# Performance work log

Hardware: AMD Instinct MI355X
Metric: run time of the kernel (lower is better)

The kernel has to match this reference:

```python
import jax, jax.numpy as jnp
import numpy as np

_EPSILON = 1e-6

def _sparsemax(z):
    # sparsemax along last axis. z: [b, m]
    z_sorted = -jnp.sort(-z, axis=-1)                       # descending sort
    m = z.shape[-1]
    k = jnp.arange(1, m + 1, dtype=z.dtype)                 # [m]
    z_cumsum = jnp.cumsum(z_sorted, axis=-1)                # [b, m]
    support = (1.0 + k * z_sorted) > z_cumsum               # [b, m] bool
    k_z = jnp.sum(support, axis=-1, keepdims=True)          # [b, 1] int, size of support
    cs_at_k = jnp.take_along_axis(z_cumsum, k_z - 1, axis=-1)
    tau = (cs_at_k - 1.0) / k_z.astype(z.dtype)             # threshold
    return jnp.maximum(z - tau, 0.0)


def setup_inputs() -> dict:
    key = jax.random.key(0)
    ks = jax.random.split(key, 6)
    b, m, dim, out_dim = 4096, 8192, 1024, 1000
    encoder_output = jax.random.normal(ks[0], (b, dim), dtype=jnp.float32)
    memory_set = jax.random.normal(ks[1], (m, dim), dtype=jnp.float32)
    loss_weights = jax.random.uniform(ks[2], (m, 1), dtype=jnp.float32)
    # classifier: Linear(2*dim, 4*dim) -> ReLU -> Linear(4*dim, out_dim)
    W1 = jax.random.normal(ks[3], (4 * dim, 2 * dim), dtype=jnp.float32) * (1.0 / np.sqrt(2 * dim))
    b1 = jnp.zeros((4 * dim,), dtype=jnp.float32)
    W2 = jax.random.normal(ks[4], (out_dim, 4 * dim), dtype=jnp.float32) * (1.0 / np.sqrt(4 * dim))
    b2 = jnp.zeros((out_dim,), dtype=jnp.float32)
    return {"encoder_output": encoder_output, "memory_set": memory_set,
            "loss_weights": loss_weights, "W1": W1, "b1": b1, "W2": W2, "b2": b2}


def reference(encoder_output, memory_set, loss_weights, W1, b1, W2, b2):
    # cosine distance: d = 1 - x_norm @ y_norm^T
    x_norm = encoder_output * jax.lax.rsqrt(
        jnp.sum(encoder_output * encoder_output, axis=1, keepdims=True) + _EPSILON)
    y_norm = memory_set * jax.lax.rsqrt(
        jnp.sum(memory_set * memory_set, axis=1, keepdims=True) + _EPSILON)
    d = 1.0 - jnp.matmul(x_norm, y_norm.T)                  # [b, m]
    content_weights = _sparsemax(-d)                        # [b, m], sparse rows
    memory_vector = jnp.matmul(content_weights, memory_set) # [b, dim]
    final_input = jnp.concatenate([encoder_output, memory_vector], axis=1)  # [b, 2*dim]
    h = jax.nn.relu(jnp.matmul(final_input, W1.T) + b1)
    output = jnp.matmul(h, W2.T) + b2                       # [b, out_dim]
    return output
```

## Files before the change

### kernel.cpp

```cpp
#include <hip/hip_runtime.h>

typedef __bf16 bf16;
typedef __bf16 bf16x4 __attribute__((ext_vector_type(4)));
typedef __bf16 bf16x8 __attribute__((ext_vector_type(8)));
typedef float f32x4 __attribute__((ext_vector_type(4)));
typedef _Float16 f16x8 __attribute__((ext_vector_type(8)));

#define WS_OFF_S    (0ull)
#define WS_OFF_PAIR (67108864ull)
#define WS_OFF_MB   (134217728ull)
#define WS_OFF_W1B  (150994944ull)
#define WS_OFF_W2B  (167772160ull)
#define WS_OFF_FI   (176160768ull)
#define WS_OFF_XN   (192937984ull)
#define WS_OFF_YN   (201326592ull)
#define WS_OFF_H    (0ull)
#define K_MAX 4095

__device__ __forceinline__ void gload_lds16(const void* g, void* l) {
  __builtin_amdgcn_global_load_lds(
      (const __attribute__((address_space(1))) void*)g,
      (__attribute__((address_space(3))) void*)l, 16, 0, 0);
}

template<int EPI>
__global__ __launch_bounds__(256)
void gemm_nt(const bf16* __restrict__ A, const bf16* __restrict__ B,
             void* __restrict__ Cout, const float* __restrict__ bias,
             int K, int ldc, int colLimit)
{
  __shared__ alignas(16) bf16 As[128 * 64];
  __shared__ alignas(16) bf16 Bs[128 * 64];
  const int tid  = threadIdx.x;
  const int lane = tid & 63;
  const int wave = tid >> 6;
  const int wr = wave >> 1, wc = wave & 1;
  const int bm0 = blockIdx.y << 7;
  const int bn0 = blockIdx.x << 7;

  const int lr   = lane >> 3;
  const int lcb  = (lane & 7) << 4;
  const int scolb = lcb ^ (lr << 4);
  const int row0 = (wave << 5) + lr;
  const char* Ag = (const char*)(A + (size_t)(bm0 + row0) * K) + scolb;
  const char* Bg = (const char*)(B + (size_t)(bn0 + row0) * K) + scolb;
  char* Al = (char*)As + (wave << 12);
  char* Bl = (char*)Bs + (wave << 12);
  const size_t rstride8 = (size_t)16 * K;

  int offA[2][4], offB[2][4];
  const int kb = (lane >> 4) << 4;
#pragma unroll
  for (int m = 0; m < 4; ++m) {
    const int rA = (wr << 6) + (m << 4) + (lane & 15);
    const int rB = (wc << 6) + (m << 4) + (lane & 15);
#pragma unroll
    for (int ks = 0; ks < 2; ++ks) {
      offA[ks][m] = (rA << 7) + ((((ks << 6) + kb)) ^ ((rA & 7) << 4));
      offB[ks][m] = (rB << 7) + ((((ks << 6) + kb)) ^ ((rB & 7) << 4));
    }
  }

  f32x4 acc[4][4];
#pragma unroll
  for (int m = 0; m < 4; ++m)
#pragma unroll
    for (int n = 0; n < 4; ++n) acc[m][n] = (f32x4)(0.0f);

  const char* Asb = (const char*)As;
  const char* Bsb = (const char*)Bs;
  const int nk = K >> 6;
  for (int kt = 0; kt < nk; ++kt) {
#pragma unroll
    for (int i = 0; i < 4; ++i) gload_lds16(Ag + i * rstride8, Al + (i << 10));
#pragma unroll
    for (int i = 0; i < 4; ++i) gload_lds16(Bg + i * rstride8, Bl + (i << 10));
    Ag += 128; Bg += 128;
    __syncthreads();
#pragma unroll
    for (int ks = 0; ks < 2; ++ks) {
      bf16x8 av[4], bv[4];
#pragma unroll
      for (int m = 0; m < 4; ++m) av[m] = *(const bf16x8*)(Asb + offA[ks][m]);
#pragma unroll
      for (int n = 0; n < 4; ++n) bv[n] = *(const bf16x8*)(Bsb + offB[ks][n]);
#pragma unroll
      for (int m = 0; m < 4; ++m)
#pragma unroll
        for (int n = 0; n < 4; ++n)
          acc[m][n] = __builtin_amdgcn_mfma_f32_16x16x32_bf16(av[m], bv[n], acc[m][n], 0, 0, 0);
    }
    __syncthreads();
  }

  const int r0 = bm0 + (wr << 6) + ((lane >> 4) << 2);
  const int c0 = bn0 + (wc << 6) + (lane & 15);
#pragma unroll
  for (int m = 0; m < 4; ++m) {
#pragma unroll
    for (int n = 0; n < 4; ++n) {
      const int col = c0 + (n << 4);
#pragma unroll
      for (int j = 0; j < 4; ++j) {
        const int row = r0 + (m << 4) + j;
        const float v = acc[m][n][j];
        if (EPI == 0) {
          ((_Float16*)Cout)[(size_t)row * ldc + col] = (_Float16)v;
        } else if (EPI == 2) {
          float t = v + bias[col];
          t = t > 0.f ? t : 0.f;
          ((bf16*)Cout)[(size_t)row * ldc + col] = (bf16)t;
        } else {
          if (col < colLimit)
            ((float*)Cout)[(size_t)row * ldc + col] = v + bias[col];
        }
      }
    }
  }
}

__global__ __launch_bounds__(256)
void rownorm_kernel(const float* __restrict__ X, bf16* __restrict__ XN,
                    bf16* __restrict__ RAW, int ldraw)
{
  const int row = blockIdx.x;
  const int tid = threadIdx.x;
  const float4 v = ((const float4*)(X + (size_t)row * 1024))[tid];
  float ss = v.x * v.x + v.y * v.y + v.z * v.z + v.w * v.w;
#pragma unroll
  for (int o = 32; o > 0; o >>= 1) ss += __shfl_down(ss, o);
  __shared__ float red[4];
  if ((tid & 63) == 0) red[tid >> 6] = ss;
  __syncthreads();
  const float rn = rsqrtf(red[0] + red[1] + red[2] + red[3] + 1e-6f);
  union { bf16 h[4]; unsigned long long u; } p;
  p.h[0] = (bf16)(v.x * rn); p.h[1] = (bf16)(v.y * rn);
  p.h[2] = (bf16)(v.z * rn); p.h[3] = (bf16)(v.w * rn);
  ((unsigned long long*)(XN + (size_t)row * 1024))[tid] = p.u;
  if (RAW != nullptr) {
    union { bf16 h[4]; unsigned long long u; } q;
    q.h[0] = (bf16)v.x; q.h[1] = (bf16)v.y; q.h[2] = (bf16)v.z; q.h[3] = (bf16)v.w;
    ((unsigned long long*)(RAW + (size_t)row * ldraw))[tid] = q.u;
  }
}

__global__ void cvt_bf16_kernel(const float* __restrict__ src, bf16* __restrict__ dst, int n4) {
  const int i = blockIdx.x * blockDim.x + threadIdx.x;
  if (i >= n4) return;
  const float4 v = ((const float4*)src)[i];
  union { bf16 h[4]; unsigned long long u; } p;
  p.h[0] = (bf16)v.x; p.h[1] = (bf16)v.y; p.h[2] = (bf16)v.z; p.h[3] = (bf16)v.w;
  ((unsigned long long*)dst)[i] = p.u;
}

__global__ void cvt_w2_kernel(const float* __restrict__ src, bf16* __restrict__ dst) {
  const int i = blockIdx.x * blockDim.x + threadIdx.x;
  const int row = i >> 10;
  union { bf16 h[4]; unsigned long long u; } p;
  if (row < 1000) {
    const float4 v = ((const float4*)src)[i];
    p.h[0] = (bf16)v.x; p.h[1] = (bf16)v.y; p.h[2] = (bf16)v.z; p.h[3] = (bf16)v.w;
  } else {
    p.u = 0ull;
  }
  ((unsigned long long*)dst)[i] = p.u;
}

__global__ __launch_bounds__(256)
void sparsemax_compact_kernel(const _Float16* __restrict__ S, unsigned* __restrict__ PAIRS)
{
  const int row = blockIdx.x;
  const int tid = threadIdx.x;
  const f16x8* zs = (const f16x8*)(S + (size_t)row * 8192);
  float z[32];
  float lsum = 0.f;
#pragma unroll
  for (int t = 0; t < 4; ++t) {
    const f16x8 v = zs[t * 256 + tid];
#pragma unroll
    for (int j = 0; j < 8; ++j) { const float f = (float)v[j]; z[t * 8 + j] = f; lsum += f; }
  }
  __shared__ float redS[4], redC[4];
  __shared__ int lcnt;
  if (tid == 0) lcnt = 0;
  float s = lsum;
#pragma unroll
  for (int o = 32; o > 0; o >>= 1) s += __shfl_down(s, o);
  if ((tid & 63) == 0) redS[tid >> 6] = s;
  __syncthreads();
  float tau = (redS[0] + redS[1] + redS[2] + redS[3] - 1.0f) * (1.0f / 8192.0f);

  for (int it = 0; it < 64; ++it) {
    float ls = 0.f, lc = 0.f;
#pragma unroll
    for (int j = 0; j < 32; ++j) {
      const float v = z[j];
      if (v > tau) { ls += v; lc += 1.0f; }
    }
#pragma unroll
    for (int o = 32; o > 0; o >>= 1) { ls += __shfl_down(ls, o); lc += __shfl_down(lc, o); }
    __syncthreads();
    if ((tid & 63) == 0) { redS[tid >> 6] = ls; redC[tid >> 6] = lc; }
    __syncthreads();
    const float Ssum = redS[0] + redS[1] + redS[2] + redS[3];
    const float Csum = redC[0] + redC[1] + redC[2] + redC[3];
    const float ntau = (Ssum - 1.0f) / Csum;
    if (!(ntau > tau)) break;
    tau = ntau;
  }

  unsigned* pr = PAIRS + ((size_t)row << 12);
#pragma unroll
  for (int t = 0; t < 4; ++t) {
#pragma unroll
    for (int j = 0; j < 8; ++j) {
      const float w = z[t * 8 + j] - tau;
      if (w > 0.f) {
        const int slot = atomicAdd(&lcnt, 1);
        if (slot < K_MAX) {
          union { _Float16 h; unsigned short us; } cv; cv.h = (_Float16)w;
          const unsigned idx = (unsigned)((t * 256 + tid) * 8 + j);
          pr[slot] = ((unsigned)cv.us << 16) | idx;
        }
      }
    }
  }
  __syncthreads();
  if (tid == 0) pr[K_MAX] = (unsigned)min(lcnt, K_MAX);
}

__global__ __launch_bounds__(256)
void gather_memvec_kernel(const unsigned* __restrict__ PAIRS, const bf16* __restrict__ MB,
                          bf16* __restrict__ FI)
{
  const int row = blockIdx.x;
  const int tid = threadIdx.x;
  const unsigned* pr = PAIRS + ((size_t)row << 12);
  const int cnt = (int)pr[K_MAX];
  __shared__ unsigned pbuf[256];
  float4 acc = make_float4(0.f, 0.f, 0.f, 0.f);
  for (int base = 0; base < cnt; base += 256) {
    const int nb = min(256, cnt - base);
    __syncthreads();
    if (tid < nb) pbuf[tid] = pr[base + tid];
    __syncthreads();
    for (int e = 0; e < nb; ++e) {
      const unsigned pk = pbuf[e];
      union { unsigned short us; _Float16 h; } cv; cv.us = (unsigned short)(pk >> 16);
      const float w = (float)cv.h;
      const size_t idx = (size_t)(pk & 0xffffu);
      const bf16x4 v = ((const bf16x4*)(MB + (idx << 10)))[tid];
      acc.x += w * (float)v[0];
      acc.y += w * (float)v[1];
      acc.z += w * (float)v[2];
      acc.w += w * (float)v[3];
    }
  }
  union { bf16 h[4]; unsigned long long u; } p;
  p.h[0] = (bf16)acc.x; p.h[1] = (bf16)acc.y; p.h[2] = (bf16)acc.z; p.h[3] = (bf16)acc.w;
  ((unsigned long long*)(FI + (size_t)row * 2048 + 1024))[tid] = p.u;
}

extern "C" void kernel_launch(void* const* d_in, const int* in_sizes, int n_in,
                              void* d_out, int out_size, void* d_ws, size_t ws_size,
                              hipStream_t stream)
{
  const float* enc = (const float*)d_in[0];
  const float* mem = (const float*)d_in[1];
  const float* W1  = (const float*)d_in[3];
  const float* b1  = (const float*)d_in[4];
  const float* W2  = (const float*)d_in[5];
  const float* b2  = (const float*)d_in[6];
  float* out = (float*)d_out;
  char* ws = (char*)d_ws;

  _Float16* S = (_Float16*)(ws + WS_OFF_S);
  unsigned* PAIRS = (unsigned*)(ws + WS_OFF_PAIR);
  bf16* MB  = (bf16*)(ws + WS_OFF_MB);
  bf16* W1B = (bf16*)(ws + WS_OFF_W1B);
  bf16* W2B = (bf16*)(ws + WS_OFF_W2B);
  bf16* FI  = (bf16*)(ws + WS_OFF_FI);
  bf16* XN  = (bf16*)(ws + WS_OFF_XN);
  bf16* YN  = (bf16*)(ws + WS_OFF_YN);
  bf16* H   = (bf16*)(ws + WS_OFF_H);

  rownorm_kernel<<<4096, 256, 0, stream>>>(enc, XN, FI, 2048);
  rownorm_kernel<<<8192, 256, 0, stream>>>(mem, YN, MB, 1024);
  cvt_bf16_kernel<<<8192, 256, 0, stream>>>(W1, W1B, 2097152);
  cvt_w2_kernel<<<4096, 256, 0, stream>>>(W2, W2B);

  gemm_nt<0><<<dim3(64, 32), 256, 0, stream>>>(XN, YN, S, nullptr, 1024, 8192, 0);
  sparsemax_compact_kernel<<<4096, 256, 0, stream>>>(S, PAIRS);
  gather_memvec_kernel<<<4096, 256, 0, stream>>>(PAIRS, MB, FI);
  gemm_nt<2><<<dim3(32, 32), 256, 0, stream>>>(FI, W1B, H, b1, 2048, 4096, 0);
  gemm_nt<3><<<dim3(8, 32), 256, 0, stream>>>(H, W2B, out, b2, 4096, 1000, 1000);
}
```

Measured before the change: 505.9 us.

## Fuse sparsemax with gather via LDS buffer and split-K the final GEMM

Merges the sparsemax threshold/compaction kernel with the memory-vector gather, so the (weight, index) pairs stay in a shared-memory buffer of 1024 entries. Multiple passes run when the support is larger than that, which removes the global PAIRS write/read and one launch. The last GEMM (only 256 blocks) is split 4-way along K through blockIdx.z to raise occupancy. Partial sums go to a workspace and a new reduce kernel sums them and adds the bias. The cost is an extra 64MB of partial-sum traffic plus the reduce launch.

```diff
diff --git a/kernel.cpp b/kernel.cpp
--- a/kernel.cpp
+++ b/kernel.cpp
@@ -7,7 +7,7 @@
 typedef _Float16 f16x8 __attribute__((ext_vector_type(8)));
 
 #define WS_OFF_S    (0ull)
-#define WS_OFF_PAIR (67108864ull)
+#define WS_OFF_P4   (67108864ull)
 #define WS_OFF_MB   (134217728ull)
 #define WS_OFF_W1B  (150994944ull)
 #define WS_OFF_W2B  (167772160ull)
@@ -15,7 +15,6 @@
 #define WS_OFF_XN   (192937984ull)
 #define WS_OFF_YN   (201326592ull)
 #define WS_OFF_H    (0ull)
-#define K_MAX 4095
 
 __device__ __forceinline__ void gload_lds16(const void* g, void* l) {
   __builtin_amdgcn_global_load_lds(
@@ -27,7 +26,7 @@
 __global__ __launch_bounds__(256)
 void gemm_nt(const bf16* __restrict__ A, const bf16* __restrict__ B,
              void* __restrict__ Cout, const float* __restrict__ bias,
-             int K, int ldc, int colLimit)
+             int K, int ldab, int ldc)
 {
   __shared__ alignas(16) bf16 As[128 * 64];
   __shared__ alignas(16) bf16 Bs[128 * 64];
@@ -37,16 +36,17 @@
   const int wr = wave >> 1, wc = wave & 1;
   const int bm0 = blockIdx.y << 7;
   const int bn0 = blockIdx.x << 7;
+  const int zc  = blockIdx.z;
 
   const int lr   = lane >> 3;
   const int lcb  = (lane & 7) << 4;
   const int scolb = lcb ^ (lr << 4);
   const int row0 = (wave << 5) + lr;
-  const char* Ag = (const char*)(A + (size_t)(bm0 + row0) * K) + scolb;
-  const char* Bg = (const char*)(B + (size_t)(bn0 + row0) * K) + scolb;
+  const char* Ag = (const char*)(A + (size_t)(bm0 + row0) * ldab + (size_t)zc * K) + scolb;
+  const char* Bg = (const char*)(B + (size_t)(bn0 + row0) * ldab + (size_t)zc * K) + scolb;
   char* Al = (char*)As + (wave << 12);
   char* Bl = (char*)Bs + (wave << 12);
-  const size_t rstride8 = (size_t)16 * K;
+  const size_t rstride8 = (size_t)16 * ldab;
 
   int offA[2][4], offB[2][4];
   const int kb = (lane >> 4) << 4;
@@ -111,12 +111,32 @@
           t = t > 0.f ? t : 0.f;
           ((bf16*)Cout)[(size_t)row * ldc + col] = (bf16)t;
         } else {
-          if (col < colLimit)
-            ((float*)Cout)[(size_t)row * ldc + col] = v + bias[col];
+          ((float*)Cout)[((size_t)zc << 22) + (size_t)row * ldc + col] = v;
         }
       }
     }
   }
+}
+
+__global__ __launch_bounds__(256)
+void reduce_bias_kernel(const float* __restrict__ P4, const float* __restrict__ b2,
+                        float* __restrict__ out)
+{
+  const int row = blockIdx.x;
+  const int t = threadIdx.x;
+  if (t >= 250) return;
+  const size_t base = (size_t)row * 1024 + (t << 2);
+  const float4 p0 = *(const float4*)(P4 + base);
+  const float4 p1 = *(const float4*)(P4 + base + (1ull << 22));
+  const float4 p2 = *(const float4*)(P4 + base + (2ull << 22));
+  const float4 p3 = *(const float4*)(P4 + base + (3ull << 22));
+  const float4 bb = ((const float4*)b2)[t];
+  float4 r;
+  r.x = p0.x + p1.x + p2.x + p3.x + bb.x;
+  r.y = p0.y + p1.y + p2.y + p3.y + bb.y;
+  r.z = p0.z + p1.z + p2.z + p3.z + bb.z;
+  r.w = p0.w + p1.w + p2.w + p3.w + bb.w;
+  *(float4*)(out + (size_t)row * 1000 + (t << 2)) = r;
 }
 
 __global__ __launch_bounds__(256)
@@ -166,8 +186,10 @@
   ((unsigned long long*)dst)[i] = p.u;
 }
 
+#define LCAP 1024
 __global__ __launch_bounds__(256)
-void sparsemax_compact_kernel(const _Float16* __restrict__ S, unsigned* __restrict__ PAIRS)
+void sparsemax_gather_kernel(const _Float16* __restrict__ S, const bf16* __restrict__ MB,
+                             bf16* __restrict__ FI)
 {
   const int row = blockIdx.x;
   const int tid = threadIdx.x;
@@ -181,8 +203,8 @@
     for (int j = 0; j < 8; ++j) { const float f = (float)v[j]; z[t * 8 + j] = f; lsum += f; }
   }
   __shared__ float redS[4], redC[4];
+  __shared__ unsigned pbuf[LCAP];
   __shared__ int lcnt;
-  if (tid == 0) lcnt = 0;
   float s = lsum;
 #pragma unroll
   for (int o = 32; o > 0; o >>= 1) s += __shfl_down(s, o);
@@ -209,41 +231,29 @@
     tau = ntau;
   }
 
-  unsigned* pr = PAIRS + ((size_t)row << 12);
-#pragma unroll
-  for (int t = 0; t < 4; ++t) {
-#pragma unroll
-    for (int j = 0; j < 8; ++j) {
-      const float w = z[t * 8 + j] - tau;
-      if (w > 0.f) {
-        const int slot = atomicAdd(&lcnt, 1);
-        if (slot < K_MAX) {
-          union { _Float16 h; unsigned short us; } cv; cv.h = (_Float16)w;
-          const unsigned idx = (unsigned)((t * 256 + tid) * 8 + j);
-          pr[slot] = ((unsigned)cv.us << 16) | idx;
-        }
+  unsigned pend = 0;
+#pragma unroll
+  for (int j = 0; j < 32; ++j)
+    if (z[j] > tau) pend |= (1u << j);
+
+  float4 acc = make_float4(0.f, 0.f, 0.f, 0.f);
+  for (;;) {
+    if (tid == 0) lcnt = 0;
+    __syncthreads();
+    unsigned rem = pend;
+    while (rem) {
+      const int j = __ffs(rem) - 1;
+      rem &= rem - 1;
+      const int slot = atomicAdd(&lcnt, 1);
+      if (slot < LCAP) {
+        union { _Float16 h; unsigned short us; } cv; cv.h = (_Float16)(z[j] - tau);
+        const unsigned idx = (unsigned)(((j >> 3) * 256 + tid) * 8 + (j & 7));
+        pbuf[slot] = ((unsigned)cv.us << 16) | idx;
+        pend &= ~(1u << j);
       }
     }
-  }
-  __syncthreads();
-  if (tid == 0) pr[K_MAX] = (unsigned)min(lcnt, K_MAX);
-}
-
-__global__ __launch_bounds__(256)
-void gather_memvec_kernel(const unsigned* __restrict__ PAIRS, const bf16* __restrict__ MB,
-                          bf16* __restrict__ FI)
-{
-  const int row = blockIdx.x;
-  const int tid = threadIdx.x;
-  const unsigned* pr = PAIRS + ((size_t)row << 12);
-  const int cnt = (int)pr[K_MAX];
-  __shared__ unsigned pbuf[256];
-  float4 acc = make_float4(0.f, 0.f, 0.f, 0.f);
-  for (int base = 0; base < cnt; base += 256) {
-    const int nb = min(256, cnt - base);
-    __syncthreads();
-    if (tid < nb) pbuf[tid] = pr[base + tid];
-    __syncthreads();
+    __syncthreads();
+    const int nb = min(lcnt, LCAP);
     for (int e = 0; e < nb; ++e) {
       const unsigned pk = pbuf[e];
       union { unsigned short us; _Float16 h; } cv; cv.us = (unsigned short)(pk >> 16);
@@ -255,7 +265,9 @@
       acc.z += w * (float)v[2];
       acc.w += w * (float)v[3];
     }
-  }
+    if (!__syncthreads_or(pend != 0)) break;
+  }
+
   union { bf16 h[4]; unsigned long long u; } p;
   p.h[0] = (bf16)acc.x; p.h[1] = (bf16)acc.y; p.h[2] = (bf16)acc.z; p.h[3] = (bf16)acc.w;
   ((unsigned long long*)(FI + (size_t)row * 2048 + 1024))[tid] = p.u;
@@ -275,7 +287,7 @@
   char* ws = (char*)d_ws;
 
   _Float16* S = (_Float16*)(ws + WS_OFF_S);
-  unsigned* PAIRS = (unsigned*)(ws + WS_OFF_PAIR);
+  float* P4 = (float*)(ws + WS_OFF_P4);
   bf16* MB  = (bf16*)(ws + WS_OFF_MB);
   bf16* W1B = (bf16*)(ws + WS_OFF_W1B);
   bf16* W2B = (bf16*)(ws + WS_OFF_W2B);
@@ -289,9 +301,9 @@
   cvt_bf16_kernel<<<8192, 256, 0, stream>>>(W1, W1B, 2097152);
   cvt_w2_kernel<<<4096, 256, 0, stream>>>(W2, W2B);
 
-  gemm_nt<0><<<dim3(64, 32), 256, 0, stream>>>(XN, YN, S, nullptr, 1024, 8192, 0);
-  sparsemax_compact_kernel<<<4096, 256, 0, stream>>>(S, PAIRS);
-  gather_memvec_kernel<<<4096, 256, 0, stream>>>(PAIRS, MB, FI);
-  gemm_nt<2><<<dim3(32, 32), 256, 0, stream>>>(FI, W1B, H, b1, 2048, 4096, 0);
-  gemm_nt<3><<<dim3(8, 32), 256, 0, stream>>>(H, W2B, out, b2, 4096, 1000, 1000);
-}
+  gemm_nt<0><<<dim3(64, 32), 256, 0, stream>>>(XN, YN, S, nullptr, 1024, 1024, 8192);
+  sparsemax_gather_kernel<<<4096, 256, 0, stream>>>(S, MB, FI);
+  gemm_nt<2><<<dim3(32, 32), 256, 0, stream>>>(FI, W1B, H, b1, 2048, 2048, 4096);
+  gemm_nt<4><<<dim3(8, 32, 4), 256, 0, stream>>>(H, W2B, P4, nullptr, 1024, 4096, 1024);
+  reduce_bias_kernel<<<4096, 256, 0, stream>>>(P4, b2, out);
+}
```

Measured after the change: 468.4 us. -7.4%, faster.
